# Kernel optimization log

Measured on AMD Instinct MI355X. Metric: run time of the kernel, lower is better.

The kernel has to match this reference:

```python
import jax, jax.numpy as jnp
import numpy as np

D_MODEL = 1024
NUM_HEADS = 16
D_K = D_MODEL // NUM_HEADS


def setup_inputs() -> dict:
    key = jax.random.key(0)
    ks = jax.random.split(key, 11)
    B, S = 4, 2048
    scale = 1.0 / np.sqrt(D_MODEL)
    inp = {
        'query': jax.random.normal(ks[0], (B, S, D_MODEL), jnp.float32),
        'key': jax.random.normal(ks[1], (B, S, D_MODEL), jnp.float32),
        'value': jax.random.normal(ks[2], (B, S, D_MODEL), jnp.float32),
        'Wq': jax.random.normal(ks[3], (D_MODEL, D_MODEL), jnp.float32) * scale,
        'bq': jnp.zeros((D_MODEL,), jnp.float32),
        'Wk': jax.random.normal(ks[4], (D_MODEL, D_MODEL), jnp.float32) * scale,
        'bk': jnp.zeros((D_MODEL,), jnp.float32),
        'Wv': jax.random.normal(ks[5], (D_MODEL, D_MODEL), jnp.float32) * scale,
        'bv': jnp.zeros((D_MODEL,), jnp.float32),
        'Wo': jax.random.normal(ks[6], (D_MODEL, D_MODEL), jnp.float32) * scale,
        'bo': jnp.zeros((D_MODEL,), jnp.float32),
    }
    return inp


def _split_heads(x):
    # [B, S, D] -> [B, H, S, d_k]
    B, S, _ = x.shape
    return x.reshape(B, S, NUM_HEADS, D_K).transpose(0, 2, 1, 3)


def reference(query, key, value, Wq, bq, Wk, bk, Wv, bv, Wo, bo):
    # torch nn.Linear: y = x @ W.T + b
    q = _split_heads(query @ Wq.T + bq)   # [B,H,Sq,dk]
    k = _split_heads(key @ Wk.T + bk)     # [B,H,Sk,dk]
    v = _split_heads(value @ Wv.T + bv)   # [B,H,Sk,dk]
    scores = jnp.einsum('bhqd,bhkd->bhqk', q, k) / jnp.sqrt(jnp.float32(D_K))
    attn = jax.nn.softmax(scores, axis=-1)
    out = jnp.einsum('bhqk,bhkd->bhqd', attn, v)  # [B,H,Sq,dk]
    B, H, Sq, dk = out.shape
    out = out.transpose(0, 2, 1, 3).reshape(B, Sq, D_MODEL)
    return out @ Wo.T + bo
```

## Files before the change

kernel.cpp:

```cpp
#include <hip/hip_runtime.h>

typedef short bf16x8 __attribute__((ext_vector_type(8)));
typedef float f32x4 __attribute__((ext_vector_type(4)));
typedef unsigned short u16;

#define S_LEN 2048
#define DM 1024
#define NH 16
#define DK 64
#define BHD ((size_t)S_LEN * DK)

#define QSCALE 0.18033688011112042f

static __device__ __forceinline__ u16 f2bf(float f) {
  union { float f; unsigned u; } x; x.f = f;
  unsigned r = x.u + 0x7FFFu + ((x.u >> 16) & 1u);
  return (u16)(r >> 16);
}

static __device__ __forceinline__ void gload_lds16(const u16* g, u16* l) {
  __builtin_amdgcn_global_load_lds(
      (const __attribute__((address_space(1))) unsigned int*)g,
      (__attribute__((address_space(3))) unsigned int*)l, 16, 0, 0);
}

__global__ __launch_bounds__(256) void conv_all(
    const float* __restrict__ q, const float* __restrict__ k, const float* __restrict__ v,
    const float* __restrict__ Wq, const float* __restrict__ Wk,
    const float* __restrict__ Wv, const float* __restrict__ Wo,
    u16* __restrict__ xq, u16* __restrict__ xk, u16* __restrict__ xv,
    u16* __restrict__ wb) {
  const int b = blockIdx.x;
  const float* s; u16* d; float sc = 1.0f; int i;
  if (b < 8192) {
    s = q; d = xq; sc = QSCALE; i = b * 256 + threadIdx.x;
  } else if (b < 16384) {
    s = k; d = xk; i = (b - 8192) * 256 + threadIdx.x;
  } else if (b < 24576) {
    s = v; d = xv; i = (b - 16384) * 256 + threadIdx.x;
  } else {
    int b2 = b - 24576, wsel = b2 >> 10;
    s = (wsel == 0) ? Wq : (wsel == 1) ? Wk : (wsel == 2) ? Wv : Wo;
    d = wb + (size_t)wsel * 1048576;
    i = (b2 & 1023) * 256 + threadIdx.x;
  }
  float4 vv = ((const float4*)s)[i];
  ushort4 h;
  h.x = f2bf(vv.x * sc); h.y = f2bf(vv.y * sc);
  h.z = f2bf(vv.z * sc); h.w = f2bf(vv.w * sc);
  ((ushort4*)d)[i] = h;
}

#define GSTAGE(DST, SRC)                                                          \
  {                                                                               \
    _Pragma("unroll") for (int j = 0; j < 4; ++j) {                               \
      gload_lds16((SRC) + (size_t)(j * 32 + (w << 3) + (l >> 3)) * 1024 +         \
                      (size_t)(((l & 7) ^ (l >> 3)) * 8),                         \
                  (DST) + (j * 256 + w * 64) * 8);                                \
    }                                                                             \
  }

__global__ __launch_bounds__(256) void proj_gemm(
    const u16* __restrict__ xq, const u16* __restrict__ xk, const u16* __restrict__ xv,
    const u16* __restrict__ wb,
    const float* __restrict__ bq, const float* __restrict__ bk, const float* __restrict__ bv,
    u16* __restrict__ qws, u16* __restrict__ kws, u16* __restrict__ vws)
{
  __shared__ u16 Al[128 * 64];
  __shared__ u16 Bl[128 * 64];
  const int z = blockIdx.z;
  const u16* Xb = (z == 0) ? xq : (z == 1) ? xk : xv;
  const u16* Wb = wb + (size_t)z * 1048576;
  const float* bias = (z == 0) ? bq : (z == 1) ? bk : bv;
  const float bscale = (z == 0) ? QSCALE : 1.0f;

  const int t = threadIdx.x;
  const int l = t & 63, w = t >> 6;
  const int lr = l & 15, lg = l >> 4;
  const int wm = w >> 1, wn = w & 1;
  const int m0 = blockIdx.x * 128, n0 = blockIdx.y * 128;
  const int sxr = lr & 7;

  f32x4 acc[4][4] = {};
  for (int k0 = 0; k0 < DM; k0 += 64) {
    __syncthreads();
    GSTAGE(Al, Xb + (size_t)m0 * 1024 + k0)
    GSTAGE(Bl, Wb + (size_t)n0 * 1024 + k0)
    __syncthreads();

    bf16x8 a[4][2], b[4][2];
#pragma unroll
    for (int mi = 0; mi < 4; ++mi) {
      const u16* rp = Al + (wm * 64 + mi * 16 + lr) * 64;
      a[mi][0] = *(const bf16x8*)(rp + ((lg ^ sxr) * 8));
      a[mi][1] = *(const bf16x8*)(rp + (((4 + lg) ^ sxr) * 8));
    }
#pragma unroll
    for (int ni = 0; ni < 4; ++ni) {
      const u16* rp = Bl + (wn * 64 + ni * 16 + lr) * 64;
      b[ni][0] = *(const bf16x8*)(rp + ((lg ^ sxr) * 8));
      b[ni][1] = *(const bf16x8*)(rp + (((4 + lg) ^ sxr) * 8));
    }
    __builtin_amdgcn_s_setprio(1);
#pragma unroll
    for (int mi = 0; mi < 4; ++mi)
#pragma unroll
      for (int ni = 0; ni < 4; ++ni) {
        acc[mi][ni] = __builtin_amdgcn_mfma_f32_16x16x32_bf16(a[mi][0], b[ni][0], acc[mi][ni], 0, 0, 0);
        acc[mi][ni] = __builtin_amdgcn_mfma_f32_16x16x32_bf16(a[mi][1], b[ni][1], acc[mi][ni], 0, 0, 0);
      }
    __builtin_amdgcn_s_setprio(0);
  }

#pragma unroll
  for (int mi = 0; mi < 4; ++mi) {
#pragma unroll
    for (int ni = 0; ni < 4; ++ni) {
#pragma unroll
      for (int r = 0; r < 4; ++r) {
        int m = m0 + wm * 64 + mi * 16 + lg * 4 + r;
        int n = n0 + wn * 64 + ni * 16 + lr;
        float y = acc[mi][ni][r] + bias[n] * bscale;
        u16 h = f2bf(y);
        int b_ = m >> 11, s = m & 2047, hh = n >> 6, d = n & 63;
        size_t head = (size_t)(b_ * NH + hh);
        if (z == 0)      qws[head * BHD + (size_t)s * DK + d] = h;
        else if (z == 1) kws[head * BHD + (size_t)s * DK + d] = h;
        else             vws[head * BHD + (size_t)d * S_LEN + s] = h;
      }
    }
  }
}

__global__ __launch_bounds__(256) void oproj_gemm(
    const u16* __restrict__ Ab, const u16* __restrict__ Wob,
    const float* __restrict__ bo, float* __restrict__ out)
{
  __shared__ u16 Al[128 * 64];
  __shared__ u16 Bl[128 * 64];
  const int t = threadIdx.x;
  const int l = t & 63, w = t >> 6;
  const int lr = l & 15, lg = l >> 4;
  const int wm = w >> 1, wn = w & 1;
  const int m0 = blockIdx.x * 128, n0 = blockIdx.y * 128;
  const int sxr = lr & 7;

  f32x4 acc[4][4] = {};
  for (int k0 = 0; k0 < DM; k0 += 64) {
    __syncthreads();
    GSTAGE(Al, Ab + (size_t)m0 * 1024 + k0)
    GSTAGE(Bl, Wob + (size_t)n0 * 1024 + k0)
    __syncthreads();

    bf16x8 a[4][2], b[4][2];
#pragma unroll
    for (int mi = 0; mi < 4; ++mi) {
      const u16* rp = Al + (wm * 64 + mi * 16 + lr) * 64;
      a[mi][0] = *(const bf16x8*)(rp + ((lg ^ sxr) * 8));
      a[mi][1] = *(const bf16x8*)(rp + (((4 + lg) ^ sxr) * 8));
    }
#pragma unroll
    for (int ni = 0; ni < 4; ++ni) {
      const u16* rp = Bl + (wn * 64 + ni * 16 + lr) * 64;
      b[ni][0] = *(const bf16x8*)(rp + ((lg ^ sxr) * 8));
      b[ni][1] = *(const bf16x8*)(rp + (((4 + lg) ^ sxr) * 8));
    }
    __builtin_amdgcn_s_setprio(1);
#pragma unroll
    for (int mi = 0; mi < 4; ++mi)
#pragma unroll
      for (int ni = 0; ni < 4; ++ni) {
        acc[mi][ni] = __builtin_amdgcn_mfma_f32_16x16x32_bf16(a[mi][0], b[ni][0], acc[mi][ni], 0, 0, 0);
        acc[mi][ni] = __builtin_amdgcn_mfma_f32_16x16x32_bf16(a[mi][1], b[ni][1], acc[mi][ni], 0, 0, 0);
      }
    __builtin_amdgcn_s_setprio(0);
  }

#pragma unroll
  for (int mi = 0; mi < 4; ++mi) {
#pragma unroll
    for (int ni = 0; ni < 4; ++ni) {
#pragma unroll
      for (int r = 0; r < 4; ++r) {
        int m = m0 + wm * 64 + mi * 16 + lg * 4 + r;
        int n = n0 + wn * 64 + ni * 16 + lr;
        out[(size_t)m * DM + n] = acc[mi][ni][r] + bo[n];
      }
    }
  }
}

__global__ __launch_bounds__(256, 4) void attn_kernel(
    const u16* __restrict__ qh, const u16* __restrict__ kh,
    const u16* __restrict__ vt, u16* __restrict__ aout)
{
  __shared__ u16 KT[2][64 * 64];
  __shared__ u16 VT[2][64 * 64];

  const int t = threadIdx.x;
  const int l = t & 63, w = t >> 6;
  const int lr = l & 15, lg = l >> 4;

  const int bid = blockIdx.x;
  const int logical = (bid & 7) * 128 + (bid >> 3);
  const int bh = logical >> 4;
  const int qb = (logical & 15) * 128 + w * 32;

  const u16* qp = qh + (size_t)bh * BHD;
  const u16* kp = kh + (size_t)bh * BHD;
  const u16* vp = vt + (size_t)bh * BHD;
  const int sx = lr & 7;

  const int srow = t >> 3;
  const int scolS = (t & 7) ^ (srow & 7);

  bf16x8 qf[2][2];
#pragma unroll
  for (int qi = 0; qi < 2; ++qi)
#pragma unroll
    for (int c = 0; c < 2; ++c)
      qf[qi][c] = *(const bf16x8*)(qp + (size_t)(qb + qi * 16 + lr) * DK + c * 32 + lg * 8);

  bf16x8 onesf;
#pragma unroll
  for (int e = 0; e < 8; ++e) onesf[e] = (short)0x3F80;

  f32x4 acc[4][2] = {};
  f32x4 acc_l[2] = {};

#define STAGE(B, KV)                                                                  \
  {                                                                                   \
    _Pragma("unroll") for (int j = 0; j < 2; ++j) {                                   \
      gload_lds16(kp + (size_t)((KV) + j * 32 + srow) * DK + scolS * 8,               \
                  &KT[B][j * 2048 + w * 512]);                                        \
      gload_lds16(vp + (size_t)(j * 32 + srow) * S_LEN + (KV) + scolS * 8,            \
                  &VT[B][j * 2048 + w * 512]);                                        \
    }                                                                                 \
  }

  STAGE(0, 0)

  for (int i = 0; i < 32; ++i) {
    __syncthreads();
    if (i < 31) STAGE((i + 1) & 1, (i + 1) * 64)

    const u16* Kb = &KT[i & 1][0];
    const u16* Vb = &VT[i & 1][0];

    f32x4 sc[4][2] = {};
    __builtin_amdgcn_s_setprio(1);
#pragma unroll
    for (int ct = 0; ct < 4; ++ct) {
      bf16x8 k0 = *(const bf16x8*)(Kb + (ct * 16 + lr) * 64 + ((lg ^ sx) * 8));
      bf16x8 k1 = *(const bf16x8*)(Kb + (ct * 16 + lr) * 64 + (((4 + lg) ^ sx) * 8));
      sc[ct][0] = __builtin_amdgcn_mfma_f32_16x16x32_bf16(k0, qf[0][0], sc[ct][0], 0, 0, 0);
      sc[ct][0] = __builtin_amdgcn_mfma_f32_16x16x32_bf16(k1, qf[0][1], sc[ct][0], 0, 0, 0);
      sc[ct][1] = __builtin_amdgcn_mfma_f32_16x16x32_bf16(k0, qf[1][0], sc[ct][1], 0, 0, 0);
      sc[ct][1] = __builtin_amdgcn_mfma_f32_16x16x32_bf16(k1, qf[1][1], sc[ct][1], 0, 0, 0);
    }
    __builtin_amdgcn_s_setprio(0);

    unsigned cpk[2][4][2];
#pragma unroll
    for (int qi = 0; qi < 2; ++qi) {
#pragma unroll
      for (int ct = 0; ct < 4; ++ct) {
        float p0 = __builtin_amdgcn_exp2f(sc[ct][qi][0]);
        float p1 = __builtin_amdgcn_exp2f(sc[ct][qi][1]);
        float p2 = __builtin_amdgcn_exp2f(sc[ct][qi][2]);
        float p3 = __builtin_amdgcn_exp2f(sc[ct][qi][3]);
        asm("v_cvt_pk_bf16_f32 %0, %1, %2" : "=v"(cpk[qi][ct][0]) : "v"(p0), "v"(p1));
        asm("v_cvt_pk_bf16_f32 %0, %1, %2" : "=v"(cpk[qi][ct][1]) : "v"(p2), "v"(p3));
      }
    }

    bf16x8 pf[2][2];
#pragma unroll
    for (int qi = 0; qi < 2; ++qi)
#pragma unroll
      for (int kk = 0; kk < 2; ++kk) {
        unsigned a0 = cpk[qi][2 * kk][0], b0 = cpk[qi][2 * kk + 1][0];
        unsigned a1 = cpk[qi][2 * kk][1], b1 = cpk[qi][2 * kk + 1][1];
        asm("v_permlane32_swap_b32 %0, %1" : "+v"(a0), "+v"(b0));
        asm("v_permlane16_swap_b32 %0, %1" : "+v"(a0), "+v"(b0));
        asm("v_permlane32_swap_b32 %0, %1" : "+v"(a1), "+v"(b1));
        asm("v_permlane16_swap_b32 %0, %1" : "+v"(a1), "+v"(b1));
        union { unsigned u[4]; bf16x8 v; } tmp;
        tmp.u[0] = a0; tmp.u[1] = a1; tmp.u[2] = b0; tmp.u[3] = b1;
        pf[qi][kk] = tmp.v;
      }

    __builtin_amdgcn_s_setprio(1);
    acc_l[0] = __builtin_amdgcn_mfma_f32_16x16x32_bf16(pf[0][0], onesf, acc_l[0], 0, 0, 0);
    acc_l[0] = __builtin_amdgcn_mfma_f32_16x16x32_bf16(pf[0][1], onesf, acc_l[0], 0, 0, 0);
    acc_l[1] = __builtin_amdgcn_mfma_f32_16x16x32_bf16(pf[1][0], onesf, acc_l[1], 0, 0, 0);
    acc_l[1] = __builtin_amdgcn_mfma_f32_16x16x32_bf16(pf[1][1], onesf, acc_l[1], 0, 0, 0);
#pragma unroll
    for (int ni = 0; ni < 4; ++ni) {
      bf16x8 vf0 = *(const bf16x8*)(Vb + (ni * 16 + lr) * 64 + ((lg ^ sx) * 8));
      bf16x8 vf1 = *(const bf16x8*)(Vb + (ni * 16 + lr) * 64 + (((4 + lg) ^ sx) * 8));
      acc[ni][0] = __builtin_amdgcn_mfma_f32_16x16x32_bf16(pf[0][0], vf0, acc[ni][0], 0, 0, 0);
      acc[ni][0] = __builtin_amdgcn_mfma_f32_16x16x32_bf16(pf[0][1], vf1, acc[ni][0], 0, 0, 0);
      acc[ni][1] = __builtin_amdgcn_mfma_f32_16x16x32_bf16(pf[1][0], vf0, acc[ni][1], 0, 0, 0);
      acc[ni][1] = __builtin_amdgcn_mfma_f32_16x16x32_bf16(pf[1][1], vf1, acc[ni][1], 0, 0, 0);
    }
    __builtin_amdgcn_s_setprio(0);
  }
#undef STAGE

  const int b_ = bh >> 4, hh = bh & 15;
#pragma unroll
  for (int qi = 0; qi < 2; ++qi) {
#pragma unroll
    for (int r = 0; r < 4; ++r) {
      float inv = 1.0f / acc_l[qi][r];
      int s = qb + qi * 16 + lg * 4 + r;
#pragma unroll
      for (int ni = 0; ni < 4; ++ni)
        aout[((size_t)(b_ * S_LEN + s)) * DM + hh * DK + ni * 16 + lr] =
            f2bf(acc[ni][qi][r] * inv);
    }
  }
}

extern "C" void kernel_launch(void* const* d_in, const int* in_sizes, int n_in,
                              void* d_out, int out_size, void* d_ws, size_t ws_size,
                              hipStream_t stream) {
  (void)in_sizes; (void)n_in; (void)out_size; (void)ws_size;
  const float* q  = (const float*)d_in[0];
  const float* k  = (const float*)d_in[1];
  const float* v  = (const float*)d_in[2];
  const float* Wq = (const float*)d_in[3];
  const float* bq = (const float*)d_in[4];
  const float* Wk = (const float*)d_in[5];
  const float* bk = (const float*)d_in[6];
  const float* Wv = (const float*)d_in[7];
  const float* bv = (const float*)d_in[8];
  const float* Wo = (const float*)d_in[9];
  const float* bo = (const float*)d_in[10];
  float* out = (float*)d_out;

  u16* qws = (u16*)d_ws;
  u16* kws = qws + (size_t)8388608;
  u16* vws = kws + (size_t)8388608;
  u16* xb  = vws + (size_t)8388608;
  u16* wb  = xb  + (size_t)8388608;
  u16* aws = xb;
  u16* kxb = (u16*)d_out;
  u16* vxb = kxb + (size_t)8388608;

  conv_all<<<dim3(28672), dim3(256), 0, stream>>>(q, k, v, Wq, Wk, Wv, Wo, xb, kxb, vxb, wb);

  proj_gemm<<<dim3(64, 8, 3), dim3(256), 0, stream>>>(xb, kxb, vxb, wb, bq, bk, bv,
                                                      qws, kws, vws);

  attn_kernel<<<dim3(1024), dim3(256), 0, stream>>>(qws, kws, vws, aws);

  oproj_gemm<<<dim3(64, 8), dim3(256), 0, stream>>>(aws, wb + 3145728, bo, out);
}
```

Baseline: 202.0 us.

## Double-buffer LDS tiles in projection GEMMs to overlap loads with MFMA

Both the QKV projection GEMM and the output projection GEMM now keep two LDS buffers per operand. The next K-tile is prefetched with global_load_lds while MFMAs run on the current tile, and the loop needs one barrier per iteration instead of two. The aim is to hide global-load latency behind compute. In exchange, LDS use per block doubles to 64KB, which can lower occupancy. The compiler may also insert vmcnt waits before the LDS reads, which would limit the overlap.

```diff
diff --git a/kernel.cpp b/kernel.cpp
--- a/kernel.cpp
+++ b/kernel.cpp
@@ -66,8 +66,8 @@
     const float* __restrict__ bq, const float* __restrict__ bk, const float* __restrict__ bv,
     u16* __restrict__ qws, u16* __restrict__ kws, u16* __restrict__ vws)
 {
-  __shared__ u16 Al[128 * 64];
-  __shared__ u16 Bl[128 * 64];
+  __shared__ u16 Al[2][128 * 64];
+  __shared__ u16 Bl[2][128 * 64];
   const int z = blockIdx.z;
   const u16* Xb = (z == 0) ? xq : (z == 1) ? xk : xv;
   const u16* Wb = wb + (size_t)z * 1048576;
@@ -82,22 +82,29 @@
   const int sxr = lr & 7;
 
   f32x4 acc[4][4] = {};
-  for (int k0 = 0; k0 < DM; k0 += 64) {
+
+  GSTAGE(&Al[0][0], Xb + (size_t)m0 * 1024)
+  GSTAGE(&Bl[0][0], Wb + (size_t)n0 * 1024)
+
+  for (int i = 0; i < 16; ++i) {
     __syncthreads();
-    GSTAGE(Al, Xb + (size_t)m0 * 1024 + k0)
-    GSTAGE(Bl, Wb + (size_t)n0 * 1024 + k0)
-    __syncthreads();
+    if (i < 15) {
+      GSTAGE(&Al[(i + 1) & 1][0], Xb + (size_t)m0 * 1024 + (i + 1) * 64)
+      GSTAGE(&Bl[(i + 1) & 1][0], Wb + (size_t)n0 * 1024 + (i + 1) * 64)
+    }
+    const u16* Ab_ = &Al[i & 1][0];
+    const u16* Bb_ = &Bl[i & 1][0];
 
     bf16x8 a[4][2], b[4][2];
 #pragma unroll
     for (int mi = 0; mi < 4; ++mi) {
-      const u16* rp = Al + (wm * 64 + mi * 16 + lr) * 64;
+      const u16* rp = Ab_ + (wm * 64 + mi * 16 + lr) * 64;
       a[mi][0] = *(const bf16x8*)(rp + ((lg ^ sxr) * 8));
       a[mi][1] = *(const bf16x8*)(rp + (((4 + lg) ^ sxr) * 8));
     }
 #pragma unroll
     for (int ni = 0; ni < 4; ++ni) {
-      const u16* rp = Bl + (wn * 64 + ni * 16 + lr) * 64;
+      const u16* rp = Bb_ + (wn * 64 + ni * 16 + lr) * 64;
       b[ni][0] = *(const bf16x8*)(rp + ((lg ^ sxr) * 8));
       b[ni][1] = *(const bf16x8*)(rp + (((4 + lg) ^ sxr) * 8));
     }
@@ -136,8 +143,8 @@
     const u16* __restrict__ Ab, const u16* __restrict__ Wob,
     const float* __restrict__ bo, float* __restrict__ out)
 {
-  __shared__ u16 Al[128 * 64];
-  __shared__ u16 Bl[128 * 64];
+  __shared__ u16 Al[2][128 * 64];
+  __shared__ u16 Bl[2][128 * 64];
   const int t = threadIdx.x;
   const int l = t & 63, w = t >> 6;
   const int lr = l & 15, lg = l >> 4;
@@ -146,22 +153,29 @@
   const int sxr = lr & 7;
 
   f32x4 acc[4][4] = {};
-  for (int k0 = 0; k0 < DM; k0 += 64) {
+
+  GSTAGE(&Al[0][0], Ab + (size_t)m0 * 1024)
+  GSTAGE(&Bl[0][0], Wob + (size_t)n0 * 1024)
+
+  for (int i = 0; i < 16; ++i) {
     __syncthreads();
-    GSTAGE(Al, Ab + (size_t)m0 * 1024 + k0)
-    GSTAGE(Bl, Wob + (size_t)n0 * 1024 + k0)
-    __syncthreads();
+    if (i < 15) {
+      GSTAGE(&Al[(i + 1) & 1][0], Ab + (size_t)m0 * 1024 + (i + 1) * 64)
+      GSTAGE(&Bl[(i + 1) & 1][0], Wob + (size_t)n0 * 1024 + (i + 1) * 64)
+    }
+    const u16* Ab_ = &Al[i & 1][0];
+    const u16* Bb_ = &Bl[i & 1][0];
 
     bf16x8 a[4][2], b[4][2];
 #pragma unroll
     for (int mi = 0; mi < 4; ++mi) {
-      const u16* rp = Al + (wm * 64 + mi * 16 + lr) * 64;
+      const u16* rp = Ab_ + (wm * 64 + mi * 16 + lr) * 64;
       a[mi][0] = *(const bf16x8*)(rp + ((lg ^ sxr) * 8));
       a[mi][1] = *(const bf16x8*)(rp + (((4 + lg) ^ sxr) * 8));
     }
 #pragma unroll
     for (int ni = 0; ni < 4; ++ni) {
-      const u16* rp = Bl + (wn * 64 + ni * 16 + lr) * 64;
+      const u16* rp = Bb_ + (wn * 64 + ni * 16 + lr) * 64;
       b[ni][0] = *(const bf16x8*)(rp + ((lg ^ sxr) * 8));
       b[ni][1] = *(const bf16x8*)(rp + (((4 + lg) ^ sxr) * 8));
     }
```

Measured after the change: 198.4 us. About the same (-1.8%).
